# Performance work log

Hardware: AMD Instinct MI355X
Metric: run time of the kernel (lower is better)

The kernel has to match this reference:

```python
import jax, jax.numpy as jnp
import numpy as np

N_NODES = 50000


def gcn_conv_max(x, edge_index, edge_weight, W, b):
    """PyG GCNConv with aggr='max': gcn_norm (add self-loops, symmetric
    degree normalization), linear transform, gather-scale-scatter_max, bias."""
    n = x.shape[0]
    row, col = edge_index[0], edge_index[1]
    loop = jnp.arange(n)
    row = jnp.concatenate([row, loop])  # sources (incl. self-loops)
    col = jnp.concatenate([col, loop])  # targets
    ew = jnp.concatenate([edge_weight, jnp.ones((n,), x.dtype)])
    deg = jax.ops.segment_sum(ew, col, num_segments=n)
    dis = jnp.where(deg > 0, jax.lax.rsqrt(deg), jnp.zeros_like(deg))
    norm = dis[row] * ew * dis[col]  # [E+N]
    h = x @ W                         # [N, out]
    msg = norm[:, None] * h[row]      # gather + scale, [E+N, out]
    agg = jax.ops.segment_max(msg, col, num_segments=n)  # scatter-max
    return agg + b


def setup_inputs() -> dict:
    key = jax.random.key(0)
    ks = jax.random.split(key, 9)
    N, E = N_NODES, 1_600_000
    x = jax.random.normal(ks[0], (N, 5), dtype=jnp.float32)
    edge_index = jax.random.randint(ks[1], (2, E), 0, N, dtype=jnp.int64)
    edge_weight = jax.random.uniform(ks[2], (E,), dtype=jnp.float32)
    s1 = 1.0 / np.sqrt(5.0)
    s2 = 1.0 / np.sqrt(240.0)
    W1 = jax.random.uniform(ks[3], (5, 240), jnp.float32, -s1, s1)
    b1 = jnp.zeros((240,), jnp.float32)
    W2 = jax.random.uniform(ks[4], (240, 240), jnp.float32, -s2, s2)
    b2 = jnp.zeros((240,), jnp.float32)
    We = jax.random.uniform(ks[5], (240, 80), jnp.float32, -s2, s2)
    be = jnp.zeros((80,), jnp.float32)
    return {"x": x, "edge_index": edge_index, "edge_weight": edge_weight,
            "W1": W1, "b1": b1, "W2": W2, "b2": b2, "We": We, "be": be}


def reference(x, edge_index, edge_weight, W1, b1, W2, b2, We, be):
    h = gcn_conv_max(x, edge_index, edge_weight, W1, b1)
    h = jax.nn.relu(h)
    h = gcn_conv_max(h, edge_index, edge_weight, W2, b2)
    h = jax.nn.relu(h)
    return h @ We + be  # [N, 80]
```

## Files before the change

### kernel.cpp

```cpp
#include <hip/hip_runtime.h>
#include <cfloat>

#define HID 240

static inline size_t alignUp(size_t x, size_t a){ return (x + a - 1) / a * a; }

typedef __bf16 bf16x8 __attribute__((ext_vector_type(8)));
typedef unsigned short u16x8 __attribute__((ext_vector_type(8)));
typedef float  f32x16 __attribute__((ext_vector_type(16)));

__device__ __forceinline__ float b2f(unsigned short u){
    return __uint_as_float(((unsigned)u) << 16);
}
__device__ __forceinline__ unsigned short f2b_rne(float f){
    unsigned r = __float_as_uint(f);
    r += 0x7FFFu + ((r >> 16) & 1u);
    return (unsigned short)(r >> 16);
}

__global__ void k_deg_hist(const int* __restrict__ col, const float* __restrict__ ew,
                           unsigned long long* __restrict__ pk,
                           unsigned* __restrict__ rank, int E){
    int e = blockIdx.x * blockDim.x + threadIdx.x;
    if (e < E){
        int c = col[e];
        unsigned q = __float2uint_rn(ew[e] * 1048576.0f);
        unsigned long long old = atomicAdd(&pk[c], (1ull << 40) | (unsigned long long)q);
        rank[e] = (unsigned)(old >> 40);
    }
}

__global__ void k_dis_bsum(const unsigned long long* __restrict__ pk,
                           float* __restrict__ dis, unsigned* __restrict__ cnt,
                           unsigned* __restrict__ bsum, int N){
    int b = blockIdx.x;
    int i = b * 256 + threadIdx.x;
    unsigned v = 0u;
    if (i < N){
        unsigned long long p = pk[i];
        unsigned c = (unsigned)(p >> 40);
        cnt[i] = c;
        float deg = 1.0f + (float)(p & 0xFFFFFFFFFFull) * (1.0f / 1048576.0f);
        dis[i] = rsqrtf(deg);
        v = (c + 32u) >> 5;
    }
    #pragma unroll
    for (int o = 32; o > 0; o >>= 1) v += __shfl_down(v, (unsigned)o, 64);
    __shared__ unsigned ws[4];
    int lane = threadIdx.x & 63, w = threadIdx.x >> 6;
    if (lane == 0) ws[w] = v;
    __syncthreads();
    if (threadIdx.x == 0) bsum[b] = ws[0] + ws[1] + ws[2] + ws[3];
}

__global__ void k_bscan(const unsigned* __restrict__ bsum, unsigned* __restrict__ boff,
                        unsigned* __restrict__ poff, int nb, int N){
    __shared__ unsigned s[256];
    int t = threadIdx.x;
    unsigned v = (t < nb) ? bsum[t] : 0u;
    s[t] = v;
    __syncthreads();
    for (int o = 1; o < 256; o <<= 1){
        unsigned u = (t >= o) ? s[t - o] : 0u;
        __syncthreads();
        s[t] += u;
        __syncthreads();
    }
    if (t < nb) boff[t] = s[t] - v;
    if (t == 0) poff[N] = 32u * s[nb - 1];
}

__global__ void k_offs_fill(const unsigned* __restrict__ cnt, const unsigned* __restrict__ boff,
                            const float* __restrict__ dis,
                            unsigned* __restrict__ poff, int2* __restrict__ sedge, int N){
    int b = blockIdx.x, t = threadIdx.x;
    int i = b * 256 + t;
    unsigned c = (i < N) ? cnt[i] : 0u;
    unsigned v = (i < N) ? ((c + 32u) >> 5) : 0u;
    int lane = t & 63, w = t >> 6;
    unsigned x = v;
    #pragma unroll
    for (int o = 1; o < 64; o <<= 1){
        unsigned u = __shfl_up(x, (unsigned)o, 64);
        if (lane >= o) x += u;
    }
    __shared__ unsigned ws[4];
    if (lane == 63) ws[w] = x;
    __syncthreads();
    unsigned wb = 0;
    if (w > 0) wb += ws[0];
    if (w > 1) wb += ws[1];
    if (w > 2) wb += ws[2];
    if (i < N){
        unsigned p = 32u * (boff[b] + wb + x - v);
        poff[i] = p;
        float dd = dis[i];
        int2 sv = make_int2(i, __float_as_int(dd * dd));
        sedge[p] = sv;
        unsigned s1 = p + 32u * v;
        for (unsigned s = p + 1u + c; s < s1; s++) sedge[s] = sv;
    }
}

__global__ void k_scatter(const int* __restrict__ row, const int* __restrict__ col,
                          const float* __restrict__ ew, const float* __restrict__ dis,
                          const unsigned* __restrict__ poff, const unsigned* __restrict__ rank,
                          int2* __restrict__ sedge, int E){
    int e = blockIdx.x * blockDim.x + threadIdx.x;
    if (e < E){
        int r = row[e], c = col[e];
        float nw = dis[r] * ew[e] * dis[c];
        unsigned p = poff[c] + 1u + rank[e];
        sedge[p] = make_int2(r, __float_as_int(nw));
    }
}

__global__ void k_prep_all(const float* __restrict__ x, float* __restrict__ xp, int N, int nbx,
                           const float* __restrict__ W1, unsigned short* __restrict__ W1f,
                           const float* __restrict__ W2, unsigned short* __restrict__ Bt2h,
                           unsigned short* __restrict__ Bt2l,
                           const float* __restrict__ We, unsigned short* __restrict__ Bt3h,
                           unsigned short* __restrict__ Bt3l){
    int b = blockIdx.x;
    int t = threadIdx.x;
    if (b < nbx){
        __shared__ float s[1280];
        int rbase = b * 256;
        #pragma unroll
        for (int c = 0; c < 5; c++){
            int idx = rbase * 5 + t + 256 * c;
            s[t + 256 * c] = (idx < N * 5) ? x[idx] : 0.0f;
        }
        __syncthreads();
        #pragma unroll
        for (int c = 0; c < 8; c++){
            int pos = t + 256 * c;
            int r = pos >> 3, j = pos & 7;
            int grow = rbase + r;
            if (grow < N)
                xp[(size_t)grow * 8 + j] = (j < 5) ? s[r * 5 + j] : 0.0f;
        }
        return;
    }
    int bb = b - nbx;
    if (bb < 32){
        int i = bb * 256 + t;
        if (i < 2 * 8 * 64 * 8){
            int k    = i & 7;
            int lane = (i >> 3) & 63;
            int j    = (i >> 9) & 7;
            int s2   = i >> 12;
            int lm = lane & 31, quad = lane >> 5;
            int kg = quad * 8 + k;
            int colm = 32 * j + lm;
            float v = (kg < 5 && colm < HID) ? W1[kg * HID + colm] : 0.0f;
            unsigned short hi = f2b_rne(v);
            W1f[i] = (s2 == 0) ? hi : f2b_rne(v - b2f(hi));
        }
        return;
    }
    bb -= 32;
    if (bb < 240){
        int i = bb * 256 + t;
        int n = i / HID, k = i - n * HID;
        float v = (n < HID) ? W2[(size_t)k * HID + n] : 0.0f;
        unsigned short hi = f2b_rne(v);
        Bt2h[i] = hi;
        Bt2l[i] = f2b_rne(v - b2f(hi));
        return;
    }
    bb -= 240;
    {
        int i = bb * 256 + t;
        if (i < 128 * HID){
            int n = i / HID, k = i - n * HID;
            float v = (n < 80) ? We[(size_t)k * 80 + n] : 0.0f;
            unsigned short hi = f2b_rne(v);
            Bt3h[i] = hi;
            Bt3l[i] = f2b_rne(v - b2f(hi));
        }
    }
}

__global__ __launch_bounds__(256) void k_agg1m(const float* __restrict__ xp,
                                               const unsigned short* __restrict__ W1f,
                                               const unsigned* __restrict__ cnt,
                                               const unsigned* __restrict__ poff,
                                               const int2* __restrict__ sedge,
                                               const float* __restrict__ bias,
                                               float* __restrict__ out, int N, int nwaves){
    int wid  = blockIdx.x * 4 + (threadIdx.x >> 6);
    int lane = threadIdx.x & 63;
    int lm   = lane & 31;

    bf16x8 bh[8], bl[8];
    #pragma unroll
    for (int j = 0; j < 8; j++){
        bh[j] = *(const bf16x8*)(W1f + ((size_t)(0 * 8 + j) * 64 + lane) * 8);
        bl[j] = *(const bf16x8*)(W1f + ((size_t)(1 * 8 + j) * 64 + lane) * 8);
    }
    float bv[8];
    #pragma unroll
    for (int j = 0; j < 8; j++){
        int c = 32 * j + lm;
        bv[j] = (c < HID) ? bias[c] : 0.0f;
    }
    const f32x16 zv = {};

    for (int d = wid; d < N; d += nwaves){
        unsigned base = poff[d];
        unsigned nch  = (cnt[d] + 32u) >> 5;
        float m[8];
        #pragma unroll
        for (int j = 0; j < 8; j++) m[j] = -FLT_MAX;

        for (unsigned c = 0; c < nch; c++){
            u16x8 ahu = (u16x8)0, alu = (u16x8)0;
            if (lane < 32){
                int2 e = sedge[base + 32u * c + (unsigned)lm];
                float w = __int_as_float(e.y);
                const float4* xr = (const float4*)(xp + (size_t)e.x * 8);
                float4 x0 = xr[0], x1 = xr[1];
                float p[5] = {w * x0.x, w * x0.y, w * x0.z, w * x0.w, w * x1.x};
                #pragma unroll
                for (int k = 0; k < 5; k++){
                    unsigned short h = f2b_rne(p[k]);
                    ahu[k] = h;
                    alu[k] = f2b_rne(p[k] - b2f(h));
                }
            }
            bf16x8 ah = __builtin_bit_cast(bf16x8, ahu);
            bf16x8 al = __builtin_bit_cast(bf16x8, alu);
            #pragma unroll
            for (int j = 0; j < 8; j += 2){
                f32x16 a0 = __builtin_amdgcn_mfma_f32_32x32x16_bf16(ah, bh[j],     zv, 0, 0, 0);
                f32x16 a1 = __builtin_amdgcn_mfma_f32_32x32x16_bf16(ah, bh[j + 1], zv, 0, 0, 0);
                a0 = __builtin_amdgcn_mfma_f32_32x32x16_bf16(ah, bl[j],     a0, 0, 0, 0);
                a1 = __builtin_amdgcn_mfma_f32_32x32x16_bf16(ah, bl[j + 1], a1, 0, 0, 0);
                a0 = __builtin_amdgcn_mfma_f32_32x32x16_bf16(al, bh[j],     a0, 0, 0, 0);
                a1 = __builtin_amdgcn_mfma_f32_32x32x16_bf16(al, bh[j + 1], a1, 0, 0, 0);
                #pragma unroll
                for (int r = 0; r < 16; r++){
                    m[j]     = fmaxf(m[j],     a0[r]);
                    m[j + 1] = fmaxf(m[j + 1], a1[r]);
                }
            }
        }
        float o[8];
        #pragma unroll
        for (int j = 0; j < 8; j++){
            float other = __shfl_xor(m[j], 32, 64);
            o[j] = fmaxf(fmaxf(m[j], other) + bv[j], 0.0f);
        }
        if (lane < 32){
            float* orow = out + (size_t)d * HID;
            #pragma unroll
            for (int j = 0; j < 8; j++){
                int c = 32 * j + lm;
                if (c < HID) orow[c] = o[j];
            }
        }
    }
}

template <bool OB16>
__global__ __launch_bounds__(256) void k_gemm_mfma(const float* __restrict__ A,
                                                   const unsigned short* __restrict__ Bth,
                                                   const unsigned short* __restrict__ Btl,
                                                   const float* __restrict__ bias,
                                                   void* __restrict__ Cv,
                                                   int M, int Ncol, int Npad){
    __shared__ unsigned short As_hi[32][24];
    __shared__ unsigned short As_lo[32][24];
    const int K = 240;
    int t = threadIdx.x;
    int wave = t >> 6, lane = t & 63;
    int m0 = blockIdx.x * 32;
    int n0 = wave * 64;
    bool wact = n0 < Npad;

    int lm   = lane & 31;
    int quad = lane >> 5;

    f32x16 acc0 = {};
    f32x16 acc1 = {};

    for (int k0 = 0; k0 < K; k0 += 16){
        if (t < 128){
            int m = t >> 2, kq = (t & 3) * 4;
            float4 av = make_float4(0.f, 0.f, 0.f, 0.f);
            if (m0 + m < M) av = *(const float4*)(A + (size_t)(m0 + m) * K + k0 + kq);
            ushort4 hi, lo;
            hi.x = f2b_rne(av.x); lo.x = f2b_rne(av.x - b2f(hi.x));
            hi.y = f2b_rne(av.y); lo.y = f2b_rne(av.y - b2f(hi.y));
            hi.z = f2b_rne(av.z); lo.z = f2b_rne(av.z - b2f(hi.z));
            hi.w = f2b_rne(av.w); lo.w = f2b_rne(av.w - b2f(hi.w));
            *(ushort4*)&As_hi[m][kq] = hi;
            *(ushort4*)&As_lo[m][kq] = lo;
        }
        __syncthreads();
        if (wact){
            bf16x8 ah = *(const bf16x8*)&As_hi[lm][quad * 8];
            bf16x8 al = *(const bf16x8*)&As_lo[lm][quad * 8];
            size_t bo0 = (size_t)(n0 + lm) * K + k0 + quad * 8;
            size_t bo1 = (size_t)(n0 + 32 + lm) * K + k0 + quad * 8;
            bf16x8 bh0 = *(const bf16x8*)(Bth + bo0);
            bf16x8 bl0 = *(const bf16x8*)(Btl + bo0);
            bf16x8 bh1 = *(const bf16x8*)(Bth + bo1);
            bf16x8 bl1 = *(const bf16x8*)(Btl + bo1);
            acc0 = __builtin_amdgcn_mfma_f32_32x32x16_bf16(ah, bh0, acc0, 0, 0, 0);
            acc0 = __builtin_amdgcn_mfma_f32_32x32x16_bf16(ah, bl0, acc0, 0, 0, 0);
            acc0 = __builtin_amdgcn_mfma_f32_32x32x16_bf16(al, bh0, acc0, 0, 0, 0);
            acc1 = __builtin_amdgcn_mfma_f32_32x32x16_bf16(ah, bh1, acc1, 0, 0, 0);
            acc1 = __builtin_amdgcn_mfma_f32_32x32x16_bf16(ah, bl1, acc1, 0, 0, 0);
            acc1 = __builtin_amdgcn_mfma_f32_32x32x16_bf16(al, bh1, acc1, 0, 0, 0);
        }
        __syncthreads();
    }

    if (!wact) return;
    #pragma unroll
    for (int h = 0; h < 2; h++){
        int n = n0 + 32 * h + lm;
        if (n >= Ncol) continue;
        float bvv = (!OB16 && bias) ? bias[n] : 0.0f;
        #pragma unroll
        for (int r = 0; r < 16; r++){
            int m = m0 + (r & 3) + 8 * (r >> 2) + 4 * quad;
            if (m >= M) continue;
            float v = (h == 0) ? acc0[r] : acc1[r];
            if (OB16){
                ((unsigned short*)Cv)[(size_t)m * Ncol + n] = f2b_rne(v);
            } else {
                ((float*)Cv)[(size_t)m * Ncol + n] = v + bvv;
            }
        }
    }
}

__global__ __launch_bounds__(256) void k_aggb(const unsigned short* __restrict__ H2,
                                              const unsigned* __restrict__ cnt,
                                              const unsigned* __restrict__ poff,
                                              const int2* __restrict__ sedge,
                                              const float* __restrict__ bias,
                                              float* __restrict__ out, int N){
    int d    = blockIdx.x * 4 + (threadIdx.x >> 6);
    int lane = threadIdx.x & 63;
    if (d >= N) return;
    bool act = lane < 60;

    float4 m = make_float4(-FLT_MAX, -FLT_MAX, -FLT_MAX, -FLT_MAX);
    unsigned p0 = poff[d], p1 = p0 + 1u + cnt[d];
    unsigned p = p0;
    for (; p + 4 <= p1; p += 4){
        int2 e0 = sedge[p], e1 = sedge[p+1], e2 = sedge[p+2], e3 = sedge[p+3];
        if (act){
            ushort4 g0 = ((const ushort4*)(H2 + (size_t)e0.x * HID))[lane];
            ushort4 g1 = ((const ushort4*)(H2 + (size_t)e1.x * HID))[lane];
            ushort4 g2 = ((const ushort4*)(H2 + (size_t)e2.x * HID))[lane];
            ushort4 g3 = ((const ushort4*)(H2 + (size_t)e3.x * HID))[lane];
            float w0 = __int_as_float(e0.y), w1 = __int_as_float(e1.y);
            float w2 = __int_as_float(e2.y), w3 = __int_as_float(e3.y);
            m.x = fmaxf(fmaxf(m.x, w0*b2f(g0.x)), fmaxf(w1*b2f(g1.x), fmaxf(w2*b2f(g2.x), w3*b2f(g3.x))));
            m.y = fmaxf(fmaxf(m.y, w0*b2f(g0.y)), fmaxf(w1*b2f(g1.y), fmaxf(w2*b2f(g2.y), w3*b2f(g3.y))));
            m.z = fmaxf(fmaxf(m.z, w0*b2f(g0.z)), fmaxf(w1*b2f(g1.z), fmaxf(w2*b2f(g2.z), w3*b2f(g3.z))));
            m.w = fmaxf(fmaxf(m.w, w0*b2f(g0.w)), fmaxf(w1*b2f(g1.w), fmaxf(w2*b2f(g2.w), w3*b2f(g3.w))));
        }
    }
    for (; p < p1; p++){
        int2 e0 = sedge[p];
        if (act){
            ushort4 g0 = ((const ushort4*)(H2 + (size_t)e0.x * HID))[lane];
            float w0 = __int_as_float(e0.y);
            m.x = fmaxf(m.x, w0 * b2f(g0.x)); m.y = fmaxf(m.y, w0 * b2f(g0.y));
            m.z = fmaxf(m.z, w0 * b2f(g0.z)); m.w = fmaxf(m.w, w0 * b2f(g0.w));
        }
    }
    if (act){
        float4 b = ((const float4*)bias)[lane];
        float4 o;
        o.x = fmaxf(m.x + b.x, 0.0f);
        o.y = fmaxf(m.y + b.y, 0.0f);
        o.z = fmaxf(m.z + b.z, 0.0f);
        o.w = fmaxf(m.w + b.w, 0.0f);
        ((float4*)(out + (size_t)d * HID))[lane] = o;
    }
}

extern "C" void kernel_launch(void* const* d_in, const int* in_sizes, int n_in,
                              void* d_out, int out_size, void* d_ws, size_t ws_size,
                              hipStream_t stream){
    const float* x  = (const float*)d_in[0];
    const int*   ei = (const int*)  d_in[1];
    const float* ew = (const float*)d_in[2];
    const float* W1 = (const float*)d_in[3];
    const float* b1 = (const float*)d_in[4];
    const float* W2 = (const float*)d_in[5];
    const float* b2 = (const float*)d_in[6];
    const float* We = (const float*)d_in[7];
    const float* be = (const float*)d_in[8];
    float* out = (float*)d_out;

    const int N = in_sizes[0] / 5;
    const int E = in_sizes[2];
    const int* row = ei;
    const int* col = ei + E;
    const int nb = (N + 255) / 256;

    char* w = (char*)d_ws;
    size_t o = 0;
    auto alloc = [&](size_t bytes) -> void* {
        void* p = w + o;
        o = alignUp(o + bytes, 256);
        return p;
    };
    unsigned long long* pk = (unsigned long long*) alloc((size_t)N * 8);
    float*          dis   = (float*)          alloc((size_t)N * 4);
    unsigned*       cnt   = (unsigned*)       alloc((size_t)N * 4);
    unsigned*       poff  = (unsigned*)       alloc((size_t)(N + 1) * 4);
    unsigned*       bsum  = (unsigned*)       alloc((size_t)nb * 4);
    unsigned*       boff  = (unsigned*)       alloc((size_t)nb * 4);
    unsigned*       rank  = (unsigned*)       alloc((size_t)E * 4);
    int2*           sedge = (int2*)           alloc(((size_t)E + 32u * N + 64u) * 8);
    float*          xp    = (float*)          alloc((size_t)N * 8 * 4);
    unsigned short* W1f   = (unsigned short*) alloc((size_t)2 * 8 * 64 * 8 * 2);
    unsigned short* Bt2h  = (unsigned short*) alloc((size_t)256 * HID * 2);
    unsigned short* Bt2l  = (unsigned short*) alloc((size_t)256 * HID * 2);
    unsigned short* Bt3h  = (unsigned short*) alloc((size_t)128 * HID * 2);
    unsigned short* Bt3l  = (unsigned short*) alloc((size_t)128 * HID * 2);
    unsigned short* bufH2 = (unsigned short*) alloc((size_t)N * HID * 2);
    float*          bufB  = (float*)          alloc((size_t)N * HID * 4);
    (void)ws_size; (void)n_in; (void)out_size;

    int be_ = (E + 255) / 256;

    hipMemsetAsync(pk, 0, (size_t)N * 8, stream);
    k_deg_hist <<<be_, 256, 0, stream>>>(col, ew, pk, rank, E);
    k_dis_bsum <<<nb, 256, 0, stream>>>(pk, dis, cnt, bsum, N);
    k_bscan    <<<1, 256, 0, stream>>>(bsum, boff, poff, nb, N);
    k_offs_fill<<<nb, 256, 0, stream>>>(cnt, boff, dis, poff, sedge, N);
    k_scatter  <<<be_, 256, 0, stream>>>(row, col, ew, dis, poff, rank, sedge, E);
    k_prep_all <<<nb + 32 + 240 + 120, 256, 0, stream>>>(x, xp, N, nb,
                                                         W1, W1f, W2, Bt2h, Bt2l,
                                                         We, Bt3h, Bt3l);

    const int a1blocks = 768;
    k_agg1m<<<a1blocks, 256, 0, stream>>>(xp, W1f, cnt, poff, sedge, b1, bufB, N, a1blocks * 4);

    int gm = (N + 31) / 32;
    k_gemm_mfma<true><<<gm, 256, 0, stream>>>(bufB, Bt2h, Bt2l, nullptr, bufH2, N, HID, 256);
    k_aggb<<<(N + 3) / 4, 256, 0, stream>>>(bufH2, cnt, poff, sedge, b2, bufB, N);

    k_gemm_mfma<false><<<gm, 256, 0, stream>>>(bufB, Bt3h, Bt3l, be, out, N, 80, 128);
}
```

Before: 507.5 us.

## Fuse graph-build preprocessing kernels into one cooperative kernel with grid syncs

Replaces the memset plus six preprocessing kernels (degree histogram, dis/block sums, block scan, offset fill, edge scatter, weight prep) with a single cooperative kernel of 512 blocks that uses grid-wide syncs between phases. The block scan becomes a single-wave loop with carry. The aim is to remove launch overhead and inter-kernel gaps. In exchange, the grid-stride loops run with fewer threads, the scan is serialized in one wave, and grid.sync adds its own cost.

```diff
diff --git a/kernel.cpp b/kernel.cpp
--- a/kernel.cpp
+++ b/kernel.cpp
@@ -1,5 +1,8 @@
 #include <hip/hip_runtime.h>
+#include <hip/hip_cooperative_groups.h>
 #include <cfloat>
+
+namespace cg = cooperative_groups;
 
 #define HID 240
 
@@ -18,167 +21,143 @@
     return (unsigned short)(r >> 16);
 }
 
-__global__ void k_deg_hist(const int* __restrict__ col, const float* __restrict__ ew,
-                           unsigned long long* __restrict__ pk,
-                           unsigned* __restrict__ rank, int E){
-    int e = blockIdx.x * blockDim.x + threadIdx.x;
-    if (e < E){
+__global__ void k_build(const int* __restrict__ col, const float* __restrict__ ew,
+                        const int* __restrict__ row,
+                        unsigned long long* __restrict__ pk, unsigned* __restrict__ rank,
+                        float* __restrict__ dis, unsigned* __restrict__ cnt,
+                        unsigned* __restrict__ bsum, unsigned* __restrict__ boff,
+                        unsigned* __restrict__ poff, int2* __restrict__ sedge,
+                        const float* __restrict__ x, float* __restrict__ xp,
+                        const float* __restrict__ W1, unsigned short* __restrict__ W1f,
+                        const float* __restrict__ W2, unsigned short* __restrict__ Bt2h,
+                        unsigned short* __restrict__ Bt2l,
+                        const float* __restrict__ We, unsigned short* __restrict__ Bt3h,
+                        unsigned short* __restrict__ Bt3l,
+                        int N, int E, int nb){
+    cg::grid_group grid = cg::this_grid();
+    __shared__ unsigned ws[4];
+    int t = threadIdx.x;
+    int lane = t & 63, w = t >> 6;
+    int gtid = blockIdx.x * 256 + t;
+    int gsz  = gridDim.x * 256;
+
+    for (int i = gtid; i < N; i += gsz) pk[i] = 0ull;
+    grid.sync();
+
+    for (int e = gtid; e < E; e += gsz){
         int c = col[e];
         unsigned q = __float2uint_rn(ew[e] * 1048576.0f);
         unsigned long long old = atomicAdd(&pk[c], (1ull << 40) | (unsigned long long)q);
         rank[e] = (unsigned)(old >> 40);
     }
-}
-
-__global__ void k_dis_bsum(const unsigned long long* __restrict__ pk,
-                           float* __restrict__ dis, unsigned* __restrict__ cnt,
-                           unsigned* __restrict__ bsum, int N){
-    int b = blockIdx.x;
-    int i = b * 256 + threadIdx.x;
-    unsigned v = 0u;
-    if (i < N){
-        unsigned long long p = pk[i];
-        unsigned c = (unsigned)(p >> 40);
-        cnt[i] = c;
-        float deg = 1.0f + (float)(p & 0xFFFFFFFFFFull) * (1.0f / 1048576.0f);
-        dis[i] = rsqrtf(deg);
-        v = (c + 32u) >> 5;
-    }
-    #pragma unroll
-    for (int o = 32; o > 0; o >>= 1) v += __shfl_down(v, (unsigned)o, 64);
-    __shared__ unsigned ws[4];
-    int lane = threadIdx.x & 63, w = threadIdx.x >> 6;
-    if (lane == 0) ws[w] = v;
-    __syncthreads();
-    if (threadIdx.x == 0) bsum[b] = ws[0] + ws[1] + ws[2] + ws[3];
-}
-
-__global__ void k_bscan(const unsigned* __restrict__ bsum, unsigned* __restrict__ boff,
-                        unsigned* __restrict__ poff, int nb, int N){
-    __shared__ unsigned s[256];
-    int t = threadIdx.x;
-    unsigned v = (t < nb) ? bsum[t] : 0u;
-    s[t] = v;
-    __syncthreads();
-    for (int o = 1; o < 256; o <<= 1){
-        unsigned u = (t >= o) ? s[t - o] : 0u;
-        __syncthreads();
-        s[t] += u;
-        __syncthreads();
-    }
-    if (t < nb) boff[t] = s[t] - v;
-    if (t == 0) poff[N] = 32u * s[nb - 1];
-}
-
-__global__ void k_offs_fill(const unsigned* __restrict__ cnt, const unsigned* __restrict__ boff,
-                            const float* __restrict__ dis,
-                            unsigned* __restrict__ poff, int2* __restrict__ sedge, int N){
-    int b = blockIdx.x, t = threadIdx.x;
-    int i = b * 256 + t;
-    unsigned c = (i < N) ? cnt[i] : 0u;
-    unsigned v = (i < N) ? ((c + 32u) >> 5) : 0u;
-    int lane = t & 63, w = t >> 6;
-    unsigned x = v;
-    #pragma unroll
-    for (int o = 1; o < 64; o <<= 1){
-        unsigned u = __shfl_up(x, (unsigned)o, 64);
-        if (lane >= o) x += u;
-    }
-    __shared__ unsigned ws[4];
-    if (lane == 63) ws[w] = x;
-    __syncthreads();
-    unsigned wb = 0;
-    if (w > 0) wb += ws[0];
-    if (w > 1) wb += ws[1];
-    if (w > 2) wb += ws[2];
-    if (i < N){
-        unsigned p = 32u * (boff[b] + wb + x - v);
-        poff[i] = p;
-        float dd = dis[i];
-        int2 sv = make_int2(i, __float_as_int(dd * dd));
-        sedge[p] = sv;
-        unsigned s1 = p + 32u * v;
-        for (unsigned s = p + 1u + c; s < s1; s++) sedge[s] = sv;
-    }
-}
-
-__global__ void k_scatter(const int* __restrict__ row, const int* __restrict__ col,
-                          const float* __restrict__ ew, const float* __restrict__ dis,
-                          const unsigned* __restrict__ poff, const unsigned* __restrict__ rank,
-                          int2* __restrict__ sedge, int E){
-    int e = blockIdx.x * blockDim.x + threadIdx.x;
-    if (e < E){
-        int r = row[e], c = col[e];
-        float nw = dis[r] * ew[e] * dis[c];
-        unsigned p = poff[c] + 1u + rank[e];
-        sedge[p] = make_int2(r, __float_as_int(nw));
-    }
-}
-
-__global__ void k_prep_all(const float* __restrict__ x, float* __restrict__ xp, int N, int nbx,
-                           const float* __restrict__ W1, unsigned short* __restrict__ W1f,
-                           const float* __restrict__ W2, unsigned short* __restrict__ Bt2h,
-                           unsigned short* __restrict__ Bt2l,
-                           const float* __restrict__ We, unsigned short* __restrict__ Bt3h,
-                           unsigned short* __restrict__ Bt3l){
-    int b = blockIdx.x;
-    int t = threadIdx.x;
-    if (b < nbx){
-        __shared__ float s[1280];
-        int rbase = b * 256;
-        #pragma unroll
-        for (int c = 0; c < 5; c++){
-            int idx = rbase * 5 + t + 256 * c;
-            s[t + 256 * c] = (idx < N * 5) ? x[idx] : 0.0f;
-        }
-        __syncthreads();
-        #pragma unroll
-        for (int c = 0; c < 8; c++){
-            int pos = t + 256 * c;
-            int r = pos >> 3, j = pos & 7;
-            int grow = rbase + r;
-            if (grow < N)
-                xp[(size_t)grow * 8 + j] = (j < 5) ? s[r * 5 + j] : 0.0f;
-        }
-        return;
-    }
-    int bb = b - nbx;
-    if (bb < 32){
-        int i = bb * 256 + t;
-        if (i < 2 * 8 * 64 * 8){
-            int k    = i & 7;
-            int lane = (i >> 3) & 63;
-            int j    = (i >> 9) & 7;
-            int s2   = i >> 12;
-            int lm = lane & 31, quad = lane >> 5;
-            int kg = quad * 8 + k;
-            int colm = 32 * j + lm;
-            float v = (kg < 5 && colm < HID) ? W1[kg * HID + colm] : 0.0f;
-            unsigned short hi = f2b_rne(v);
-            W1f[i] = (s2 == 0) ? hi : f2b_rne(v - b2f(hi));
-        }
-        return;
-    }
-    bb -= 32;
-    if (bb < 240){
-        int i = bb * 256 + t;
+    for (int i = gtid; i < N; i += gsz){
+        const float* xr = x + (size_t)i * 5;
+        float v0 = xr[0], v1 = xr[1], v2 = xr[2], v3 = xr[3], v4 = xr[4];
+        float* o = xp + (size_t)i * 8;
+        o[0] = v0; o[1] = v1; o[2] = v2; o[3] = v3;
+        o[4] = v4; o[5] = 0.f; o[6] = 0.f; o[7] = 0.f;
+    }
+    for (int i = gtid; i < 2 * 8 * 64 * 8; i += gsz){
+        int k    = i & 7;
+        int ln   = (i >> 3) & 63;
+        int j    = (i >> 9) & 7;
+        int s2   = i >> 12;
+        int lm = ln & 31, quad = ln >> 5;
+        int kg = quad * 8 + k;
+        int colm = 32 * j + lm;
+        float v = (kg < 5 && colm < HID) ? W1[kg * HID + colm] : 0.0f;
+        unsigned short hi = f2b_rne(v);
+        W1f[i] = (s2 == 0) ? hi : f2b_rne(v - b2f(hi));
+    }
+    for (int i = gtid; i < 256 * HID; i += gsz){
         int n = i / HID, k = i - n * HID;
         float v = (n < HID) ? W2[(size_t)k * HID + n] : 0.0f;
         unsigned short hi = f2b_rne(v);
         Bt2h[i] = hi;
         Bt2l[i] = f2b_rne(v - b2f(hi));
-        return;
-    }
-    bb -= 240;
-    {
-        int i = bb * 256 + t;
-        if (i < 128 * HID){
-            int n = i / HID, k = i - n * HID;
-            float v = (n < 80) ? We[(size_t)k * 80 + n] : 0.0f;
-            unsigned short hi = f2b_rne(v);
-            Bt3h[i] = hi;
-            Bt3l[i] = f2b_rne(v - b2f(hi));
-        }
+    }
+    for (int i = gtid; i < 128 * HID; i += gsz){
+        int n = i / HID, k = i - n * HID;
+        float v = (n < 80) ? We[(size_t)k * 80 + n] : 0.0f;
+        unsigned short hi = f2b_rne(v);
+        Bt3h[i] = hi;
+        Bt3l[i] = f2b_rne(v - b2f(hi));
+    }
+    grid.sync();
+
+    for (int seg = blockIdx.x; seg < nb; seg += gridDim.x){
+        int i = seg * 256 + t;
+        unsigned v = 0u;
+        if (i < N){
+            unsigned long long p = pk[i];
+            unsigned c = (unsigned)(p >> 40);
+            cnt[i] = c;
+            float deg = 1.0f + (float)(p & 0xFFFFFFFFFFull) * (1.0f / 1048576.0f);
+            dis[i] = rsqrtf(deg);
+            v = (c + 32u) >> 5;
+        }
+        unsigned r = v;
+        #pragma unroll
+        for (int o = 32; o > 0; o >>= 1) r += __shfl_down(r, (unsigned)o, 64);
+        if (lane == 0) ws[w] = r;
+        __syncthreads();
+        if (t == 0) bsum[seg] = ws[0] + ws[1] + ws[2] + ws[3];
+        __syncthreads();
+    }
+    grid.sync();
+
+    if (blockIdx.x == 0 && t < 64){
+        unsigned carry = 0u;
+        for (int base = 0; base < nb; base += 64){
+            int i = base + lane;
+            unsigned v = (i < nb) ? bsum[i] : 0u;
+            unsigned xacc = v;
+            #pragma unroll
+            for (int o = 1; o < 64; o <<= 1){
+                unsigned u = __shfl_up(xacc, (unsigned)o, 64);
+                if (lane >= o) xacc += u;
+            }
+            if (i < nb) boff[i] = carry + xacc - v;
+            carry += __shfl(xacc, 63, 64);
+        }
+        if (lane == 0) poff[N] = 32u * carry;
+    }
+    grid.sync();
+
+    for (int seg = blockIdx.x; seg < nb; seg += gridDim.x){
+        int i = seg * 256 + t;
+        unsigned c = (i < N) ? cnt[i] : 0u;
+        unsigned v = (i < N) ? ((c + 32u) >> 5) : 0u;
+        unsigned xacc = v;
+        #pragma unroll
+        for (int o = 1; o < 64; o <<= 1){
+            unsigned u = __shfl_up(xacc, (unsigned)o, 64);
+            if (lane >= o) xacc += u;
+        }
+        if (lane == 63) ws[w] = xacc;
+        __syncthreads();
+        unsigned wb = 0;
+        if (w > 0) wb += ws[0];
+        if (w > 1) wb += ws[1];
+        if (w > 2) wb += ws[2];
+        if (i < N){
+            unsigned p = 32u * (boff[seg] + wb + xacc - v);
+            poff[i] = p;
+            float dd = dis[i];
+            int2 sv = make_int2(i, __float_as_int(dd * dd));
+            sedge[p] = sv;
+            unsigned s1 = p + 32u * v;
+            for (unsigned s = p + 1u + c; s < s1; s++) sedge[s] = sv;
+        }
+        __syncthreads();
+    }
+    grid.sync();
+
+    for (int e = gtid; e < E; e += gsz){
+        int r = row[e], c = col[e];
+        float nw = dis[r] * ew[e] * dis[c];
+        unsigned p = poff[c] + 1u + rank[e];
+        sedge[p] = make_int2(r, __float_as_int(nw));
     }
 }
 
@@ -432,17 +411,19 @@
     float*          bufB  = (float*)          alloc((size_t)N * HID * 4);
     (void)ws_size; (void)n_in; (void)out_size;
 
-    int be_ = (E + 255) / 256;
-
-    hipMemsetAsync(pk, 0, (size_t)N * 8, stream);
-    k_deg_hist <<<be_, 256, 0, stream>>>(col, ew, pk, rank, E);
-    k_dis_bsum <<<nb, 256, 0, stream>>>(pk, dis, cnt, bsum, N);
-    k_bscan    <<<1, 256, 0, stream>>>(bsum, boff, poff, nb, N);
-    k_offs_fill<<<nb, 256, 0, stream>>>(cnt, boff, dis, poff, sedge, N);
-    k_scatter  <<<be_, 256, 0, stream>>>(row, col, ew, dis, poff, rank, sedge, E);
-    k_prep_all <<<nb + 32 + 240 + 120, 256, 0, stream>>>(x, xp, N, nb,
-                                                         W1, W1f, W2, Bt2h, Bt2l,
-                                                         We, Bt3h, Bt3l);
+    {
+        void* args[] = {
+            (void*)&col, (void*)&ew, (void*)&row,
+            (void*)&pk, (void*)&rank, (void*)&dis, (void*)&cnt,
+            (void*)&bsum, (void*)&boff, (void*)&poff, (void*)&sedge,
+            (void*)&x, (void*)&xp,
+            (void*)&W1, (void*)&W1f,
+            (void*)&W2, (void*)&Bt2h, (void*)&Bt2l,
+            (void*)&We, (void*)&Bt3h, (void*)&Bt3l,
+            (void*)&N, (void*)&E, (void*)&nb
+        };
+        hipLaunchCooperativeKernel((void*)k_build, dim3(512), dim3(256), args, 0, stream);
+    }
 
     const int a1blocks = 768;
     k_agg1m<<<a1blocks, 256, 0, stream>>>(xp, W1f, cnt, poff, sedge, b1, bufB, N, a1blocks * 4);
```

New measurement: 787.7 us. 1.55x slower.
